# Kernel tuning notes

Measured on AMD Instinct MI355X. Metric: run time of the kernel, lower is better.

Reference implementation:

```python
import jax, jax.numpy as jnp
import numpy as np

DIM = 1024
HEADS = 16
DIM_HEAD = 64
INNER = HEADS * DIM_HEAD  # 1024
MLP = 4096
EPS = 1e-5


def setup_inputs() -> dict:
    key = jax.random.key(0)
    ks = jax.random.split(key, 8)
    s = lambda fan_in: 1.0 / np.sqrt(fan_in)
    return {
        "x": jax.random.normal(ks[0], (4, 2048, DIM), dtype=jnp.float32),
        "ln1_g": jnp.ones((DIM,), jnp.float32),
        "ln1_b": jnp.zeros((DIM,), jnp.float32),
        "w_qkv": jax.random.normal(ks[1], (DIM, 3 * INNER), jnp.float32) * s(DIM),
        "w_out": jax.random.normal(ks[2], (INNER, DIM), jnp.float32) * s(INNER),
        "b_out": jnp.zeros((DIM,), jnp.float32),
        "ln2_g": jnp.ones((DIM,), jnp.float32),
        "ln2_b": jnp.zeros((DIM,), jnp.float32),
        "w1": jax.random.normal(ks[3], (DIM, MLP), jnp.float32) * s(DIM),
        "b1": jnp.zeros((MLP,), jnp.float32),
        "w2": jax.random.normal(ks[4], (MLP, DIM), jnp.float32) * s(MLP),
        "b2": jnp.zeros((DIM,), jnp.float32),
    }


def _layernorm(x, g, b):
    mu = jnp.mean(x, axis=-1, keepdims=True)
    var = jnp.mean(jnp.square(x - mu), axis=-1, keepdims=True)
    return (x - mu) * jax.lax.rsqrt(var + EPS) * g + b


def _block(x, ln1_g, ln1_b, w_qkv, w_out, b_out, ln2_g, ln2_b, w1, b1, w2, b2):
    # pre-norm attention
    h = _layernorm(x, ln1_g, ln1_b)
    qkv = h @ w_qkv  # [b, n, 3*inner]
    q, k, v = jnp.split(qkv, 3, axis=-1)
    def heads(t):  # b n (h d) -> b h n d
        b, n, _ = t.shape
        return t.reshape(b, n, HEADS, DIM_HEAD).transpose(0, 2, 1, 3)
    q, k, v = heads(q), heads(k), heads(v)
    scale = DIM_HEAD ** -0.5
    dots = jnp.einsum("bhnd,bhmd->bhnm", q, k) * scale
    attn = jax.nn.softmax(dots, axis=-1)
    out = jnp.einsum("bhnm,bhmd->bhnd", attn, v)
    b, _, n, _ = out.shape
    out = out.transpose(0, 2, 1, 3).reshape(b, n, INNER)
    x = out @ w_out + b_out + x
    # pre-norm FFN
    h = _layernorm(x, ln2_g, ln2_b)
    h = jax.nn.gelu(h @ w1 + b1, approximate=False)
    return h @ w2 + b2 + x


def reference(x, ln1_g, ln1_b, w_qkv, w_out, b_out, ln2_g, ln2_b, w1, b1, w2, b2):
    return _block(x, ln1_g, ln1_b, w_qkv, w_out, b_out, ln2_g, ln2_b, w1, b1, w2, b2)
```

## Files before the change

kernel.cpp:

```cpp
#include <hip/hip_runtime.h>
#include <hip/hip_bf16.h>
#include <math.h>


typedef __bf16 bf16;
typedef __bf16 bf16x8 __attribute__((ext_vector_type(8)));
typedef __bf16 bf16x4 __attribute__((ext_vector_type(4)));
typedef float  f32x4  __attribute__((ext_vector_type(4)));
typedef unsigned int u32;

#define MFMA_16x16x32(a, b, c) __builtin_amdgcn_mfma_f32_16x16x32_bf16((a), (b), (c), 0, 0, 0)

__device__ __forceinline__ void gl_lds16(const void* g, void* l) {
    __builtin_amdgcn_global_load_lds(
        (const __attribute__((address_space(1))) u32*)g,
        (__attribute__((address_space(3))) u32*)l, 16, 0, 0);
}

__device__ __forceinline__ float fast_gelu(float x) {
    const float u = x * (0.7978845608028654f + 0.03567740814183f * x * x);
    const float e = __builtin_amdgcn_exp2f(u * 2.8853900817779268f);
    return x * e * __builtin_amdgcn_rcpf(e + 1.0f);
}

__global__ __launch_bounds__(256) void transpose_f32_bf16(
    const float* __restrict__ in, bf16* __restrict__ out, int R, int C)
{
    __shared__ float tile[32][33];
    const int cb = blockIdx.x * 32, rb = blockIdx.y * 32;
    const int c = threadIdx.x & 31, r0 = threadIdx.x >> 5;
#pragma unroll
    for (int i = 0; i < 4; ++i) {
        int r = r0 + i * 8;
        tile[r][c] = in[(size_t)(rb + r) * C + cb + c];
    }
    __syncthreads();
#pragma unroll
    for (int i = 0; i < 4; ++i) {
        int rr = r0 + i * 8;
        out[(size_t)(cb + rr) * R + rb + c] = (bf16)tile[c][rr];
    }
}

__global__ __launch_bounds__(256) void transpose_v(
    const bf16* __restrict__ qkv, bf16* __restrict__ VT)
{
    __shared__ float tile[32][33];
    const int tokb = blockIdx.x * 32;
    const int db   = blockIdx.y * 32;
    const int bh   = blockIdx.z;
    const int b = bh >> 4, h = bh & 15;
    const int c = threadIdx.x & 31, r0 = threadIdx.x >> 5;
#pragma unroll
    for (int i = 0; i < 4; ++i) {
        int r = r0 + i * 8;
        tile[r][c] = (float)qkv[(size_t)(b * 2048 + tokb + r) * 3072 + 2048 + h * 64 + db + c];
    }
    __syncthreads();
#pragma unroll
    for (int i = 0; i < 4; ++i) {
        int rr = r0 + i * 8;
        VT[((size_t)bh * 64 + db + rr) * 2048 + tokb + c] = (bf16)tile[c][rr];
    }
}

__global__ __launch_bounds__(256) void ln_kernel(
    const float* __restrict__ x, const float* __restrict__ g,
    const float* __restrict__ b, bf16* __restrict__ out)
{
    const int lane = threadIdx.x & 63;
    const int wv   = threadIdx.x >> 6;
    const size_t token = (size_t)blockIdx.x * 4 + wv;
    const float* xr = x + token * 1024;
    float4 v[4];
    float s = 0.f, ss = 0.f;
#pragma unroll
    for (int c = 0; c < 4; ++c) {
        v[c] = *(const float4*)(xr + c * 256 + lane * 4);
        s  += v[c].x + v[c].y + v[c].z + v[c].w;
        ss += v[c].x * v[c].x + v[c].y * v[c].y + v[c].z * v[c].z + v[c].w * v[c].w;
    }
#pragma unroll
    for (int off = 32; off > 0; off >>= 1) {
        s  += __shfl_xor(s, off);
        ss += __shfl_xor(ss, off);
    }
    const float mu  = s * (1.0f / 1024.0f);
    const float var = ss * (1.0f / 1024.0f) - mu * mu;
    const float rs  = rsqrtf(var + 1e-5f);
    bf16* orow = out + token * 1024;
#pragma unroll
    for (int c = 0; c < 4; ++c) {
        float4 gg = *(const float4*)(g + c * 256 + lane * 4);
        float4 bb = *(const float4*)(b + c * 256 + lane * 4);
        bf16x4 o;
        o[0] = (bf16)((v[c].x - mu) * rs * gg.x + bb.x);
        o[1] = (bf16)((v[c].y - mu) * rs * gg.y + bb.y);
        o[2] = (bf16)((v[c].z - mu) * rs * gg.z + bb.z);
        o[3] = (bf16)((v[c].w - mu) * rs * gg.w + bb.w);
        *(bf16x4*)(orow + c * 256 + lane * 4) = o;
    }
}

template <int EPI>
__global__ __launch_bounds__(256, 4) void gemm_bt(
    const bf16* __restrict__ A, const bf16* __restrict__ Bt,
    const float* __restrict__ bias, const float* __restrict__ resid,
    void* __restrict__ outp, int M, int N, int K)
{
    __shared__ __align__(16) bf16 sA[128 * 64];
    __shared__ __align__(16) bf16 sB[128 * 64];

    const int tid  = threadIdx.x;
    const int lane = tid & 63;
    const int wv   = tid >> 6;
    const int quad = lane >> 4;
    const int l16  = lane & 15;

    const int id  = blockIdx.x;
    const int xcd = id & 7, j = id >> 3;
    const int M0 = (xcd * 8 + (j & 7)) * 128;
    const int N0 = (j >> 3) * 128;

    const int wm = (wv >> 1) * 64;
    const int wn = (wv & 1) * 64;

    f32x4 acc[4][4] = {};

    const bf16* paG[4];
    const bf16* pbG[4];
#pragma unroll
    for (int c = 0; c < 4; ++c) {
        const int f = c * 256 + tid;
        const int row = f >> 3;
        const int gch = (f & 7) ^ (row & 7);
        paG[c] = A  + (size_t)(M0 + row) * K + gch * 8;
        pbG[c] = Bt + (size_t)(N0 + row) * K + gch * 8;
    }

    const int sw = l16 & 7;

    for (int k0 = 0; k0 < K; k0 += 64) {
        __syncthreads();
#pragma unroll
        for (int c = 0; c < 4; ++c) {
            const int f8 = (c * 256 + tid) * 8;
            gl_lds16(paG[c] + k0, sA + f8);
            gl_lds16(pbG[c] + k0, sB + f8);
        }
        __syncthreads();

#pragma unroll
        for (int s = 0; s < 2; ++s) {
            const int chp = (s * 4 + quad) ^ sw;
            bf16x8 af[4], bfr[4];
#pragma unroll
            for (int t = 0; t < 4; ++t)
                af[t] = *(const bf16x8*)(sA + ((wm + t * 16 + l16) << 6) + chp * 8);
#pragma unroll
            for (int t = 0; t < 4; ++t)
                bfr[t] = *(const bf16x8*)(sB + ((wn + t * 16 + l16) << 6) + chp * 8);
#pragma unroll
            for (int tm = 0; tm < 4; ++tm)
#pragma unroll
                for (int tn = 0; tn < 4; ++tn)
                    acc[tm][tn] = MFMA_16x16x32(bfr[tn], af[tm], acc[tm][tn]);
        }
    }

#pragma unroll
    for (int tm = 0; tm < 4; ++tm) {
        const int row = M0 + wm + tm * 16 + l16;
#pragma unroll
        for (int tn = 0; tn < 4; ++tn) {
            const int col = N0 + wn + tn * 16 + quad * 4;
            const size_t idx = (size_t)row * N + col;
            const f32x4 v = acc[tm][tn];
            if (EPI == 0) {
                bf16x4 o;
#pragma unroll
                for (int r = 0; r < 4; ++r) o[r] = (bf16)v[r];
                *(bf16x4*)((bf16*)outp + idx) = o;
            } else if (EPI == 1) {
                const f32x4 b4 = *(const f32x4*)(bias + col);
                const f32x4 r4 = *(const f32x4*)(resid + idx);
                *(f32x4*)((float*)outp + idx) = v + b4 + r4;
            } else {
                const f32x4 b4 = *(const f32x4*)(bias + col);
                bf16x4 o;
#pragma unroll
                for (int r = 0; r < 4; ++r) o[r] = (bf16)fast_gelu(v[r] + b4[r]);
                *(bf16x4*)((bf16*)outp + idx) = o;
            }
        }
    }
}

#define BAR256()  asm volatile("s_barrier" ::: "memory")
#define WAITVM(n) asm volatile("s_waitcnt vmcnt(" #n ")" ::: "memory")
#define WAITLG()  do { asm volatile("s_waitcnt lgkmcnt(0)" ::: "memory"); \
                       __builtin_amdgcn_sched_barrier(0); } while (0)

template <int EPI>
__global__ __launch_bounds__(512, 2) void gemm256(
    const bf16* __restrict__ A, const bf16* __restrict__ Bt,
    const float* __restrict__ bias, void* __restrict__ outp,
    int N, int K)
{
    __shared__ __align__(16) bf16 sA[2][16384];
    __shared__ __align__(16) bf16 sB[2][16384];

    const int tid  = threadIdx.x;
    const int lane = tid & 63;
    const int wv   = tid >> 6;
    const int quad = lane >> 4;
    const int l16  = lane & 15;
    const int wr   = wv >> 2;
    const int wc   = wv & 3;

    const int id = blockIdx.x;
    const int wg = (id & 7) * ((int)gridDim.x >> 3) + (id >> 3);
    const int M0 = (wg & 31) * 256;
    const int N0 = (wg >> 5) * 256;

    const int srow = tid >> 3;
    const int sch  = (tid & 7) ^ (srow & 7);
    const bf16* gA = A  + (size_t)(M0 + srow) * K + sch * 8;
    const bf16* gB = Bt + (size_t)(N0 + srow) * K + sch * 8;
    const size_t r64  = (size_t)64 * K;
    const size_t r128 = (size_t)128 * K;

    f32x4 acc[8][4] = {};
    bf16x8 af[4][2], bf0[2][2], bf1[2][2];

    auto STG = [&](const bf16* g, bf16* l) {
        gl_lds16(g, l + tid * 8);
        gl_lds16(g + r64, l + tid * 8 + 4096);
    };
    auto LDA = [&](int buf, int mh) {
#pragma unroll
        for (int tm = 0; tm < 4; ++tm) {
            const int row = wr * 128 + mh * 64 + tm * 16 + l16;
            const bf16* p = &sA[buf][row * 64];
            const int swz = (row & 7) << 3;
            af[tm][0] = *(const bf16x8*)(p + (( quad      << 3) ^ swz));
            af[tm][1] = *(const bf16x8*)(p + (((quad + 4) << 3) ^ swz));
        }
    };
    auto LDB = [&](int buf, int nh, bf16x8 (&bfr)[2][2]) {
#pragma unroll
        for (int tn = 0; tn < 2; ++tn) {
            const int row = wc * 64 + nh * 32 + tn * 16 + l16;
            const bf16* p = &sB[buf][row * 64];
            const int swz = (row & 7) << 3;
            bfr[tn][0] = *(const bf16x8*)(p + (( quad      << 3) ^ swz));
            bfr[tn][1] = *(const bf16x8*)(p + (((quad + 4) << 3) ^ swz));
        }
    };
    auto MM = [&](int mh, int nh, bf16x8 (&bfr)[2][2]) {
        __builtin_amdgcn_s_setprio(1);
#pragma unroll
        for (int tm = 0; tm < 4; ++tm)
#pragma unroll
            for (int tn = 0; tn < 2; ++tn) {
                f32x4& a = acc[mh * 4 + tm][nh * 2 + tn];
                a = MFMA_16x16x32(bfr[tn][0], af[tm][0], a);
                a = MFMA_16x16x32(bfr[tn][1], af[tm][1], a);
            }
        __builtin_amdgcn_s_setprio(0);
    };

    STG(gA,              &sA[0][0]);
    STG(gA + r128,       &sA[0][8192]);
    STG(gB,              &sB[0][0]);
    STG(gB + r128,       &sB[0][8192]);
    STG(gB + 64,         &sB[1][0]);
    STG(gB + r128 + 64,  &sB[1][8192]);
    WAITVM(4);
    BAR256();

    const int NU = K >> 7;
#pragma unroll 1
    for (int u = 0; u < NU; ++u) {
        const size_t k1 = (size_t)(2 * u + 1) * 64;
        const size_t k2 = (size_t)(2 * u + 2) * 64;
        const size_t k3 = (size_t)(2 * u + 3) * 64;
        const bool more = (u + 1 < NU);

        LDA(0, 0); LDB(0, 0, bf0);
        STG(gA + k1, &sA[1][0]);
        BAR256(); WAITLG(); MM(0, 0, bf0); BAR256();

        LDB(0, 1, bf1);
        STG(gA + r128 + k1, &sA[1][8192]);
        BAR256(); WAITLG(); MM(0, 1, bf1); BAR256();

        LDA(0, 1);
        if (more) STG(gB + k2, &sB[0][0]);
        BAR256(); WAITLG(); MM(1, 1, bf1); BAR256();

        if (more) STG(gB + r128 + k2, &sB[0][8192]);
        BAR256(); MM(1, 0, bf0);
        if (more) { WAITVM(4); } else { WAITVM(0); }
        BAR256();

        LDA(1, 0); LDB(1, 0, bf0);
        if (more) STG(gA + k2, &sA[0][0]);
        BAR256(); WAITLG(); MM(0, 0, bf0); BAR256();

        LDB(1, 1, bf1);
        if (more) STG(gA + r128 + k2, &sA[0][8192]);
        BAR256(); WAITLG(); MM(0, 1, bf1); BAR256();

        LDA(1, 1);
        if (more) STG(gB + k3, &sB[1][0]);
        BAR256(); WAITLG(); MM(1, 1, bf1); BAR256();

        if (more) {
            STG(gB + r128 + k3, &sB[1][8192]);
            BAR256(); MM(1, 0, bf0);
            WAITVM(4);
            BAR256();
        } else {
            BAR256(); MM(1, 0, bf0);
        }
    }

#pragma unroll
    for (int tm = 0; tm < 8; ++tm) {
        const int row = M0 + wr * 128 + (tm >> 2) * 64 + (tm & 3) * 16 + l16;
#pragma unroll
        for (int tn = 0; tn < 4; ++tn) {
            const int col = N0 + wc * 64 + (tn >> 1) * 32 + (tn & 1) * 16 + quad * 4;
            const size_t idx = (size_t)row * N + col;
            const f32x4 v = acc[tm][tn];
            if (EPI == 0) {
                bf16x4 o;
#pragma unroll
                for (int r = 0; r < 4; ++r) o[r] = (bf16)v[r];
                *(bf16x4*)((bf16*)outp + idx) = o;
            } else {
                const f32x4 b4 = *(const f32x4*)(bias + col);
                bf16x4 o;
#pragma unroll
                for (int r = 0; r < 4; ++r) o[r] = (bf16)fast_gelu(v[r] + b4[r]);
                *(bf16x4*)((bf16*)outp + idx) = o;
            }
        }
    }
}

__global__ __launch_bounds__(256, 4) void attn_kernel(
    const bf16* __restrict__ qkv, const bf16* __restrict__ VT,
    bf16* __restrict__ attn_out)
{
    __shared__ __align__(16) bf16 sK[4096];
    __shared__ __align__(16) bf16 sV[4096];
    __shared__ __align__(16) bf16 sP[4][32][72];

    const int bh = blockIdx.y, b = bh >> 4, h = bh & 15;
    const int tid = threadIdx.x, lane = tid & 63, wv = tid >> 6;
    const int quad = lane >> 4, l16 = lane & 15;
    const size_t tok0 = (size_t)b * 2048;
    const int q0 = blockIdx.x * 128 + wv * 32;

    bf16x8 qf[2][2];
#pragma unroll
    for (int mi = 0; mi < 2; ++mi)
#pragma unroll
        for (int c = 0; c < 2; ++c) {
            bf16x8 t = *(const bf16x8*)(qkv + (tok0 + q0 + mi * 16 + l16) * 3072 + h * 64 + c * 32 + quad * 8);
#pragma unroll
            for (int j = 0; j < 8; ++j) t[j] = (bf16)((float)t[j] * 0.18033688011112042f);
            qf[mi][c] = t;
        }

    f32x4 o[2][4] = {};
    float l[2][4] = {};

    const int fA = tid, fB = tid + 256;
    const int cKA = fA >> 8, keyA = (fA >> 2) & 63, qcA = fA & 3;
    const int cKB = fB >> 8, keyB = (fB >> 2) & 63, qcB = fB & 3;
    const int dVA = fA >> 3, ccA = fA & 7;
    const int dVB = fB >> 3, ccB = fB & 7;
    const bf16* Kb = qkv + 1024 + h * 64;
    const bf16* Vb = VT + (size_t)bh * 64 * 2048;

    for (int kt = 0; kt < 32; ++kt) {
        const int kb = kt * 64;
        __syncthreads();
        gl_lds16(Kb + (tok0 + kb + keyA) * 3072 + cKA * 32 + ((qcA ^ (keyA & 3)) * 8), sK + fA * 8);
        gl_lds16(Kb + (tok0 + kb + keyB) * 3072 + cKB * 32 + ((qcB ^ (keyB & 3)) * 8), sK + fB * 8);
        gl_lds16(Vb + (size_t)dVA * 2048 + kb + ((ccA ^ (dVA & 7)) * 8), sV + fA * 8);
        gl_lds16(Vb + (size_t)dVB * 2048 + kb + ((ccB ^ (dVB & 7)) * 8), sV + fB * 8);
        __syncthreads();

        f32x4 s[2][4];
#pragma unroll
        for (int ct = 0; ct < 4; ++ct) {
            const int key = ct * 16 + l16;
            const int ch = quad ^ (l16 & 3);
            bf16x8 k0 = *(const bf16x8*)(sK + (key * 4 + ch) * 8);
            bf16x8 k1 = *(const bf16x8*)(sK + (256 + key * 4 + ch) * 8);
#pragma unroll
            for (int mi = 0; mi < 2; ++mi) {
                f32x4 z = {};
                z = MFMA_16x16x32(qf[mi][0], k0, z);
                z = MFMA_16x16x32(qf[mi][1], k1, z);
                s[mi][ct] = z;
            }
        }
#pragma unroll
        for (int mi = 0; mi < 2; ++mi)
#pragma unroll
            for (int ct = 0; ct < 4; ++ct)
#pragma unroll
                for (int r = 0; r < 4; ++r) {
                    const float p = __builtin_amdgcn_exp2f(s[mi][ct][r]);
                    l[mi][r] += p;
                    sP[wv][mi * 16 + quad * 4 + r][ct * 16 + l16] = (bf16)p;
                }
        bf16x8 vb[4][2];
#pragma unroll
        for (int dt = 0; dt < 4; ++dt) {
            const int d = dt * 16 + l16;
            vb[dt][0] = *(const bf16x8*)(sV + (d * 8 + (quad ^ (l16 & 7))) * 8);
            vb[dt][1] = *(const bf16x8*)(sV + (d * 8 + ((quad + 4) ^ (l16 & 7))) * 8);
        }
#pragma unroll
        for (int mi = 0; mi < 2; ++mi) {
            bf16x8 p0 = *(const bf16x8*)&sP[wv][mi * 16 + l16][quad * 8];
            bf16x8 p1 = *(const bf16x8*)&sP[wv][mi * 16 + l16][32 + quad * 8];
#pragma unroll
            for (int dt = 0; dt < 4; ++dt) {
                o[mi][dt] = MFMA_16x16x32(p0, vb[dt][0], o[mi][dt]);
                o[mi][dt] = MFMA_16x16x32(p1, vb[dt][1], o[mi][dt]);
            }
        }
    }

#pragma unroll
    for (int mi = 0; mi < 2; ++mi) {
        float rl[4];
#pragma unroll
        for (int r = 0; r < 4; ++r) {
            float t = l[mi][r];
            t += __shfl_xor(t, 1); t += __shfl_xor(t, 2);
            t += __shfl_xor(t, 4); t += __shfl_xor(t, 8);
            rl[r] = 1.0f / t;
        }
#pragma unroll
        for (int dt = 0; dt < 4; ++dt)
#pragma unroll
            for (int r = 0; r < 4; ++r) {
                const size_t tok = tok0 + q0 + mi * 16 + quad * 4 + r;
                attn_out[tok * 1024 + h * 64 + dt * 16 + l16] = (bf16)(o[mi][dt][r] * rl[r]);
            }
    }
}

extern "C" void kernel_launch(void* const* d_in, const int* in_sizes, int n_in,
                              void* d_out, int out_size, void* d_ws, size_t ws_size,
                              hipStream_t stream)
{
    const float* x     = (const float*)d_in[0];
    const float* ln1_g = (const float*)d_in[1];
    const float* ln1_b = (const float*)d_in[2];
    const float* w_qkv = (const float*)d_in[3];
    const float* w_out = (const float*)d_in[4];
    const float* b_out = (const float*)d_in[5];
    const float* ln2_g = (const float*)d_in[6];
    const float* ln2_b = (const float*)d_in[7];
    const float* w1    = (const float*)d_in[8];
    const float* b1    = (const float*)d_in[9];
    const float* w2    = (const float*)d_in[10];
    const float* b2    = (const float*)d_in[11];
    float* out = (float*)d_out;

    char* ws = (char*)d_ws;
    bf16*  h      = (bf16*)(ws);
    bf16*  big    = (bf16*)(ws + 16777216);
    bf16*  attn_o = (bf16*)(ws + 83886080);
    float* x_mid  = (float*)(ws + 100663296);
    bf16*  VT     = (bf16*)(ws + 100663296);
    bf16*  wT_qkv = (bf16*)(ws + 134217728);
    bf16*  wT_out = (bf16*)(ws + 140509184);
    bf16*  wT_1   = (bf16*)(ws + 142606336);
    bf16*  wT_2   = (bf16*)(ws + 150994944);

    transpose_f32_bf16<<<dim3(3072/32, 1024/32), 256, 0, stream>>>(w_qkv, wT_qkv, 1024, 3072);
    transpose_f32_bf16<<<dim3(1024/32, 1024/32), 256, 0, stream>>>(w_out, wT_out, 1024, 1024);
    transpose_f32_bf16<<<dim3(4096/32, 1024/32), 256, 0, stream>>>(w1,    wT_1,   1024, 4096);
    transpose_f32_bf16<<<dim3(1024/32, 4096/32), 256, 0, stream>>>(w2,    wT_2,   4096, 1024);

    ln_kernel<<<2048, 256, 0, stream>>>(x, ln1_g, ln1_b, h);

    gemm256<0><<<384, 512, 0, stream>>>(h, wT_qkv, nullptr, big, 3072, 1024);

    transpose_v<<<dim3(64, 2, 64), 256, 0, stream>>>(big, VT);

    attn_kernel<<<dim3(16, 64), 256, 0, stream>>>(big, VT, attn_o);

    gemm_bt<1><<<64 * 8, 256, 0, stream>>>(attn_o, wT_out, b_out, x, x_mid, 8192, 1024, 1024);

    ln_kernel<<<2048, 256, 0, stream>>>(x_mid, ln2_g, ln2_b, h);

    gemm256<2><<<512, 512, 0, stream>>>(h, wT_1, b1, big, 4096, 1024);

    gemm_bt<1><<<64 * 8, 256, 0, stream>>>(big, wT_2, b2, x_mid, out, 8192, 1024, 4096);
}
```

Baseline: 522.7 us.

## Keep attention probabilities in registers via permlane swaps; use gemm_bt for QKV

The attention kernel now computes S^T by swapping the MFMA operands, so each lane holds the scores for one query row. After exp2 it packs them to bf16 and uses v_permlane32/16 swaps to build the P operand for the PV MFMA directly in registers. This drops the LDS round-trip through sP and simplifies the row-sum reduction. It also adds s_setprio around the MFMA sections and switches the QKV projection from gemm256 to the gemm_bt kernel, which may change GEMM efficiency either way.

```diff
diff --git a/kernel.cpp b/kernel.cpp
--- a/kernel.cpp
+++ b/kernel.cpp
@@ -6,15 +6,25 @@
 typedef __bf16 bf16;
 typedef __bf16 bf16x8 __attribute__((ext_vector_type(8)));
 typedef __bf16 bf16x4 __attribute__((ext_vector_type(4)));
+typedef __bf16 bf16x2 __attribute__((ext_vector_type(2)));
 typedef float  f32x4  __attribute__((ext_vector_type(4)));
 typedef unsigned int u32;
+typedef u32 u32x4 __attribute__((ext_vector_type(4)));
 
 #define MFMA_16x16x32(a, b, c) __builtin_amdgcn_mfma_f32_16x16x32_bf16((a), (b), (c), 0, 0, 0)
+
+#define SWAP32(x, y) asm("v_permlane32_swap_b32 %0, %1" : "+v"(x), "+v"(y))
+#define SWAP16(x, y) asm("v_permlane16_swap_b32 %0, %1" : "+v"(x), "+v"(y))
 
 __device__ __forceinline__ void gl_lds16(const void* g, void* l) {
     __builtin_amdgcn_global_load_lds(
         (const __attribute__((address_space(1))) u32*)g,
         (__attribute__((address_space(3))) u32*)l, 16, 0, 0);
+}
+
+__device__ __forceinline__ u32 pack_bf16x2(float a, float b) {
+    bf16x2 t; t[0] = (bf16)a; t[1] = (bf16)b;
+    return __builtin_bit_cast(u32, t);
 }
 
 __device__ __forceinline__ float fast_gelu(float x) {
@@ -356,7 +366,6 @@
 {
     __shared__ __align__(16) bf16 sK[4096];
     __shared__ __align__(16) bf16 sV[4096];
-    __shared__ __align__(16) bf16 sP[4][32][72];
 
     const int bh = blockIdx.y, b = bh >> 4, h = bh & 15;
     const int tid = threadIdx.x, lane = tid & 63, wv = tid >> 6;
@@ -376,7 +385,7 @@
         }
 
     f32x4 o[2][4] = {};
-    float l[2][4] = {};
+    float lsum[2] = {0.f, 0.f};
 
     const int fA = tid, fB = tid + 256;
     const int cKA = fA >> 8, keyA = (fA >> 2) & 63, qcA = fA & 3;
@@ -395,7 +404,8 @@
         gl_lds16(Vb + (size_t)dVB * 2048 + kb + ((ccB ^ (dVB & 7)) * 8), sV + fB * 8);
         __syncthreads();
 
-        f32x4 s[2][4];
+        u32 w[2][4][2];
+        __builtin_amdgcn_s_setprio(1);
 #pragma unroll
         for (int ct = 0; ct < 4; ++ct) {
             const int key = ct * 16 + l16;
@@ -405,50 +415,61 @@
 #pragma unroll
             for (int mi = 0; mi < 2; ++mi) {
                 f32x4 z = {};
-                z = MFMA_16x16x32(qf[mi][0], k0, z);
-                z = MFMA_16x16x32(qf[mi][1], k1, z);
-                s[mi][ct] = z;
-            }
-        }
-#pragma unroll
-        for (int mi = 0; mi < 2; ++mi)
-#pragma unroll
-            for (int ct = 0; ct < 4; ++ct)
-#pragma unroll
-                for (int r = 0; r < 4; ++r) {
-                    const float p = __builtin_amdgcn_exp2f(s[mi][ct][r]);
-                    l[mi][r] += p;
-                    sP[wv][mi * 16 + quad * 4 + r][ct * 16 + l16] = (bf16)p;
-                }
-        bf16x8 vb[4][2];
+                z = MFMA_16x16x32(k0, qf[mi][0], z);
+                z = MFMA_16x16x32(k1, qf[mi][1], z);
+                float p0 = __builtin_amdgcn_exp2f(z[0]);
+                float p1 = __builtin_amdgcn_exp2f(z[1]);
+                float p2 = __builtin_amdgcn_exp2f(z[2]);
+                float p3 = __builtin_amdgcn_exp2f(z[3]);
+                lsum[mi] += (p0 + p1) + (p2 + p3);
+                w[mi][ct][0] = pack_bf16x2(p0, p1);
+                w[mi][ct][1] = pack_bf16x2(p2, p3);
+            }
+        }
+        __builtin_amdgcn_s_setprio(0);
+
+        bf16x8 pa[2][2];
+#pragma unroll
+        for (int mi = 0; mi < 2; ++mi) {
+            u32 pw0[4], pw1[4];
+#pragma unroll
+            for (int c2 = 0; c2 < 2; ++c2) {
+                u32 x = w[mi][0][c2], y = w[mi][1][c2];
+                SWAP32(x, y); SWAP16(x, y);
+                pw0[c2] = x; pw0[2 + c2] = y;
+                u32 x2 = w[mi][2][c2], y2 = w[mi][3][c2];
+                SWAP32(x2, y2); SWAP16(x2, y2);
+                pw1[c2] = x2; pw1[2 + c2] = y2;
+            }
+            u32x4 t0 = {pw0[0], pw0[1], pw0[2], pw0[3]};
+            u32x4 t1 = {pw1[0], pw1[1], pw1[2], pw1[3]};
+            pa[mi][0] = __builtin_bit_cast(bf16x8, t0);
+            pa[mi][1] = __builtin_bit_cast(bf16x8, t1);
+        }
+
+        __builtin_amdgcn_s_setprio(1);
 #pragma unroll
         for (int dt = 0; dt < 4; ++dt) {
             const int d = dt * 16 + l16;
-            vb[dt][0] = *(const bf16x8*)(sV + (d * 8 + (quad ^ (l16 & 7))) * 8);
-            vb[dt][1] = *(const bf16x8*)(sV + (d * 8 + ((quad + 4) ^ (l16 & 7))) * 8);
-        }
-#pragma unroll
-        for (int mi = 0; mi < 2; ++mi) {
-            bf16x8 p0 = *(const bf16x8*)&sP[wv][mi * 16 + l16][quad * 8];
-            bf16x8 p1 = *(const bf16x8*)&sP[wv][mi * 16 + l16][32 + quad * 8];
-#pragma unroll
-            for (int dt = 0; dt < 4; ++dt) {
-                o[mi][dt] = MFMA_16x16x32(p0, vb[dt][0], o[mi][dt]);
-                o[mi][dt] = MFMA_16x16x32(p1, vb[dt][1], o[mi][dt]);
-            }
-        }
+            bf16x8 v0 = *(const bf16x8*)(sV + (d * 8 + (quad ^ (l16 & 7))) * 8);
+            bf16x8 v1 = *(const bf16x8*)(sV + (d * 8 + ((quad + 4) ^ (l16 & 7))) * 8);
+#pragma unroll
+            for (int mi = 0; mi < 2; ++mi) {
+                o[mi][dt] = MFMA_16x16x32(pa[mi][0], v0, o[mi][dt]);
+                o[mi][dt] = MFMA_16x16x32(pa[mi][1], v1, o[mi][dt]);
+            }
+        }
+        __builtin_amdgcn_s_setprio(0);
     }
 
 #pragma unroll
     for (int mi = 0; mi < 2; ++mi) {
+        float t = lsum[mi];
+        t += __shfl_xor(t, 16);
+        t += __shfl_xor(t, 32);
         float rl[4];
 #pragma unroll
-        for (int r = 0; r < 4; ++r) {
-            float t = l[mi][r];
-            t += __shfl_xor(t, 1); t += __shfl_xor(t, 2);
-            t += __shfl_xor(t, 4); t += __shfl_xor(t, 8);
-            rl[r] = 1.0f / t;
-        }
+        for (int r = 0; r < 4; ++r) rl[r] = 1.0f / __shfl(t, quad * 4 + r);
 #pragma unroll
         for (int dt = 0; dt < 4; ++dt)
 #pragma unroll
@@ -495,7 +516,7 @@
 
     ln_kernel<<<2048, 256, 0, stream>>>(x, ln1_g, ln1_b, h);
 
-    gemm256<0><<<384, 512, 0, stream>>>(h, wT_qkv, nullptr, big, 3072, 1024);
+    gemm_bt<0><<<64 * 24, 256, 0, stream>>>(h, wT_qkv, nullptr, nullptr, big, 8192, 3072, 1024);
 
     transpose_v<<<dim3(64, 2, 64), 256, 0, stream>>>(big, VT);
 
```

Result: faster. 505.8 us (-3.2%).
